# Kernel optimization log

Hardware: AMD Instinct MI355X
Metric: run time of the kernel (lower is better)

## Reference

```python
import jax, jax.numpy as jnp
import numpy as np

# module config (init_kwargs)
AH, AW = 14, 14            # aligned_height, aligned_width
SCALE = 0.25               # spatial_scale
RATIO = 2                  # sampling_ratio
SHIFT = 0.0                # spatial_shift (added in feature-map coords)
HALF_PART = 0              # 0 = full box
ROI_SCALE = 1.0            # box rescale about its center


def setup_inputs() -> dict:
    key = jax.random.key(0)
    kf, kb, kx, ky, kw, kh = jax.random.split(key, 6)
    B, C, H, W = 2, 256, 200, 272
    N = 256
    features = jax.random.normal(kf, (B, C, H, W), dtype=jnp.float32)
    img_h, img_w = H / SCALE, W / SCALE
    bidx = jax.random.randint(kb, (N,), 0, B).astype(jnp.float32)
    x1 = jax.random.uniform(kx, (N,)) * (img_w * 0.6)
    y1 = jax.random.uniform(ky, (N,)) * (img_h * 0.6)
    bw = 32.0 + jax.random.uniform(kw, (N,)) * (img_w * 0.35)
    bh = 32.0 + jax.random.uniform(kh, (N,)) * (img_h * 0.35)
    rois = jnp.stack([bidx, x1, y1, x1 + bw, y1 + bh], axis=1).astype(jnp.float32)
    return {"features": features, "rois": rois}


def _lin_idx(coord, size):
    # bilinear index/weight prep with RoIAlign boundary rules
    valid = (coord > -1.0) & (coord < float(size))
    c = jnp.clip(coord, 0.0, float(size - 1))
    lo = jnp.floor(c)
    hi = jnp.minimum(lo + 1.0, float(size - 1))
    frac = c - lo
    return lo.astype(jnp.int32), hi.astype(jnp.int32), frac, valid.astype(coord.dtype)


def _roi_mask_align(features, rois):
    B, C, H, W = features.shape
    N = rois.shape[0]
    PH, PW, r = AH + 1, AW + 1, RATIO
    b = rois[:, 0].astype(jnp.int32)
    # to feature-map coords, with roi_scale about the box center and spatial_shift
    x1, y1, x2, y2 = (rois[:, 1] * SCALE, rois[:, 2] * SCALE,
                      rois[:, 3] * SCALE, rois[:, 4] * SCALE)
    cx, cy = 0.5 * (x1 + x2), 0.5 * (y1 + y2)
    hw, hh = 0.5 * (x2 - x1) * ROI_SCALE, 0.5 * (y2 - y1) * ROI_SCALE
    x1, x2 = cx - hw + SHIFT, cx + hw + SHIFT
    y1, y2 = cy - hh + SHIFT, cy + hh + SHIFT
    roi_w = jnp.maximum(x2 - x1, 1.0)
    roi_h = jnp.maximum(y2 - y1, 1.0)
    bin_w = roi_w / PW
    bin_h = roi_h / PH
    # sample coords, separable: sx [N, PW*r], sy [N, PH*r]
    ix = jnp.arange(PW * r, dtype=jnp.float32)
    iy = jnp.arange(PH * r, dtype=jnp.float32)
    sx = x1[:, None] + (ix[None, :] + 0.5) * (bin_w[:, None] / r)
    sy = y1[:, None] + (iy[None, :] + 0.5) * (bin_h[:, None] / r)
    y_lo, y_hi, fy, vy = _lin_idx(sy, H)
    x_lo, x_hi, fx, vx = _lin_idx(sx, W)
    featsT = jnp.transpose(features, (0, 2, 3, 1))  # [B,H,W,C]
    bb = b[:, None, None]
    gather = lambda yi, xi: featsT[bb, yi[:, :, None], xi[:, None, :]]  # [N,Sy,Sx,C]
    wy0, wy1 = 1.0 - fy, fy
    wx0, wx1 = 1.0 - fx, fx
    val = (gather(y_lo, x_lo) * (wy0[:, :, None] * wx0[:, None, :])[..., None]
           + gather(y_lo, x_hi) * (wy0[:, :, None] * wx1[:, None, :])[..., None]
           + gather(y_hi, x_lo) * (wy1[:, :, None] * wx0[:, None, :])[..., None]
           + gather(y_hi, x_hi) * (wy1[:, :, None] * wx1[:, None, :])[..., None])
    val = val * (vy[:, :, None] * vx[:, None, :])[..., None]
    # average the r*r samples per bin -> [N, PH, PW, C]
    val = val.reshape(N, PH, r, PW, r, C).mean(axis=(2, 4))
    return jnp.transpose(val, (0, 3, 1, 2))  # [N, C, PH, PW]


def reference(features, rois):
    x = _roi_mask_align(features, rois)  # [N, C, AH+1, AW+1]
    # avg_pool2d(kernel=2, stride=1)
    out = 0.25 * (x[..., :-1, :-1] + x[..., 1:, :-1]
                  + x[..., :-1, 1:] + x[..., 1:, 1:])
    return out  # [N, C, AH, AW]
```

## Files before the change

### kernel.cpp

```cpp
#include <hip/hip_runtime.h>


#define AH_  14
#define AW_  14
#define C_   256
#define H_   200
#define W_   272
#define HW_  (H_ * W_)
#define CPB  4
#define WBUF 1424

#define GLOAD_LDS16(g, l)                                                     \
  __builtin_amdgcn_global_load_lds(                                           \
      (const __attribute__((address_space(1))) void*)(g),                     \
      (__attribute__((address_space(3))) void*)(l), 16, 0, 0)

__global__ __launch_bounds__(128)
void roi_mask_align_avg_kernel(const float* __restrict__ feat,
                               const float* __restrict__ rois,
                               float* __restrict__ out) {
    __shared__ float Ls[2][WBUF];

    const int p   = blockIdx.x;
    const int xcd = p & 7;
    const int q   = p >> 3;
    const int n   = q & 255;
    const int cgi = q >> 8;
    const int cg  = cgi * 8 + xcd;
    const int c0  = cg * CPB;

    const int tid  = threadIdx.x;
    const int wave = tid >> 6;
    const int lane = tid & 63;
    const int half = lane >> 5;
    const int ix   = lane & 31;

    float* __restrict__ LsW = Ls[wave];
    if (lane == 0) LsW[1024] = 0.0f;

    const float r0f = rois[n * 5 + 0];
    const float x1s = rois[n * 5 + 1] * 0.25f;
    const float y1s = rois[n * 5 + 2] * 0.25f;
    const float x2s = rois[n * 5 + 3] * 0.25f;
    const float y2s = rois[n * 5 + 4] * 0.25f;
    const int   b   = (int)r0f;

    const float cx = 0.5f * (x1s + x2s), cy = 0.5f * (y1s + y2s);
    const float hw = 0.5f * (x2s - x1s), hh = 0.5f * (y2s - y1s);
    const float x1 = cx - hw, x2 = cx + hw;
    const float y1 = cy - hh, y2 = cy + hh;
    const float roi_w = fmaxf(x2 - x1, 1.0f);
    const float roi_h = fmaxf(y2 - y1, 1.0f);
    const float sub_w = roi_w * (1.0f / 15.0f) * 0.5f;
    const float sub_h = roi_h * (1.0f / 15.0f) * 0.5f;

    const float sx  = x1 + ((float)ix + 0.5f) * sub_w;
    const bool  vx_ = (sx > -1.0f) && (sx < (float)W_) && (ix < 30);
    const float ccx = fminf(fmaxf(sx, 0.0f), (float)(W_ - 1));
    const float lox = floorf(ccx);
    const int   xl  = (int)lox;
    const int   xh  = min(xl + 1, W_ - 1);
    const float fx  = ccx - lox;
    const float vmx = vx_ ? 1.0f : 0.0f;
    const float wx0 = (1.0f - fx) * vmx;
    const float wx1 = fx * vmx;

    const int s0    = __builtin_amdgcn_readfirstlane(xl);
    const int s0c   = min(s0, W_ - 128);
    const int xh29  = __builtin_amdgcn_readlane(xh, 29);
    const int spanrel = xh29 - s0c;
    const bool ldact  = (ix * 4) <= spanrel;
    const int iA    = half * 128 + (xl - s0c);

    const float* __restrict__ bpA = feat + ((size_t)b * C_ + c0) * (size_t)HW_;
    const float* __restrict__ gA  = bpA + (size_t)half * HW_ + s0c + 4 * ix;
    const float* __restrict__ gB  = gA + 2 * HW_;

    const int  aw   = ix >> 1;
    const bool emit = ((lane & 1) == 0) && (aw < AW_);
    float* __restrict__ Ow = LsW + 1028;

    float alo0 = 0.f, alo1 = 0.f, ahi0 = 0.f, ahi1 = 0.f;
    float blo0 = 0.f, blo1 = 0.f, bhi0 = 0.f, bhi1 = 0.f;
    int   pyl = -100, pyh = -100;

    const int iy0 = wave * 14;
    float prevSA = 0.f, prevSB = 0.f;

    for (int kk = 0; kk < 8; ++kk) {
        float PA = 0.f, PB = 0.f;
        #pragma unroll
        for (int r = 0; r < 2; ++r) {
            const int iy = iy0 + 2 * kk + r;
            const float sy  = y1 + ((float)iy + 0.5f) * sub_h;
            const bool  vy_ = (sy > -1.0f) && (sy < (float)H_);
            const float ccy = fminf(fmaxf(sy, 0.0f), (float)(H_ - 1));
            const float loy = floorf(ccy);
            const float fy  = ccy - loy;
            const float vmy = vy_ ? 1.0f : 0.0f;
            const float wy0 = (1.0f - fy) * vmy;
            const float wy1 = fy * vmy;

            const int yl_s = __builtin_amdgcn_readfirstlane((int)loy);
            const int yh_s = min(yl_s + 1, H_ - 1);

            if (yl_s == pyl && yh_s == pyh) {
            } else if (yl_s == pyh) {
                alo0 = ahi0; alo1 = ahi1; blo0 = bhi0; blo1 = bhi1;
                const int ro = yh_s * W_;
                asm volatile("s_waitcnt lgkmcnt(0)" ::: "memory");
                if (ldact) {
                    GLOAD_LDS16(gA + ro, LsW + 512);
                    GLOAD_LDS16(gB + ro, LsW + 768);
                }
                asm volatile("s_waitcnt vmcnt(0)" ::: "memory");
                ahi0 = LsW[512 + iA]; ahi1 = LsW[512 + iA + 1];
                bhi0 = LsW[768 + iA]; bhi1 = LsW[768 + iA + 1];
            } else {
                const int rlo = yl_s * W_, rhi = yh_s * W_;
                asm volatile("s_waitcnt lgkmcnt(0)" ::: "memory");
                if (ldact) {
                    GLOAD_LDS16(gA + rlo, LsW + 0);
                    GLOAD_LDS16(gB + rlo, LsW + 256);
                    GLOAD_LDS16(gA + rhi, LsW + 512);
                    GLOAD_LDS16(gB + rhi, LsW + 768);
                }
                asm volatile("s_waitcnt vmcnt(0)" ::: "memory");
                alo0 = LsW[iA];       alo1 = LsW[iA + 1];
                blo0 = LsW[256 + iA]; blo1 = LsW[256 + iA + 1];
                ahi0 = LsW[512 + iA]; ahi1 = LsW[512 + iA + 1];
                bhi0 = LsW[768 + iA]; bhi1 = LsW[768 + iA + 1];
            }
            pyl = yl_s; pyh = yh_s;

            const float w00 = wy0 * wx0, w01 = wy0 * wx1;
            const float w10 = wy1 * wx0, w11 = wy1 * wx1;
            PA += alo0 * w00 + alo1 * w01 + ahi0 * w10 + ahi1 * w11;
            PB += blo0 * w00 + blo1 * w01 + bhi0 * w10 + bhi1 * w11;
        }
        const float tA = PA + __shfl_xor(PA, 1, 64);
        const float uA = tA + __shfl_down(tA, 2, 64);
        const float tB = PB + __shfl_xor(PB, 1, 64);
        const float uB = tB + __shfl_down(tB, 2, 64);
        if (kk > 0 && emit) {
            const int row = kk - 1;
            Ow[half * 98 + row * AW_ + aw]       = (prevSA + uA) * 0.0625f;
            Ow[(2 + half) * 98 + row * AW_ + aw] = (prevSB + uB) * 0.0625f;
        }
        prevSA = uA;
        prevSB = uB;
    }

    float* __restrict__ op = out + ((size_t)n * C_ + c0) * (AH_ * AW_);
    for (int o = lane; o < CPB * 7 * AW_; o += 64) {
        const int ch  = o / 98;
        const int rem = o - ch * 98;
        op[ch * (AH_ * AW_) + wave * 98 + rem] = Ow[o];
    }
}

extern "C" void kernel_launch(void* const* d_in, const int* in_sizes, int n_in,
                              void* d_out, int out_size, void* d_ws, size_t ws_size,
                              hipStream_t stream) {
    const float* feat = (const float*)d_in[0];
    const float* rois = (const float*)d_in[1];
    float* out = (float*)d_out;
    const int grid = 256 * (C_ / CPB);
    roi_mask_align_avg_kernel<<<grid, 128, 0, stream>>>(feat, rois, out);
}
```

Baseline: 233.5 us.

## Double-buffer row staging to overlap next-row global loads with current compute

Replaces the row-reuse branching loop with a fully unrolled 16-step loop. Each step prefetches the next sample row pair into an alternate LDS buffer using async global-to-LDS loads, then waits only on the older batch with vmcnt(4). Row reuse is dropped, so every sample row pair is reloaded, which adds memory traffic in exchange for hiding load latency. It also zero-fills a larger LDS region, shifts the second half-wave's load window left by 8 columns, and keeps the output rows in registers until the end.

```diff
diff --git a/kernel.cpp b/kernel.cpp
--- a/kernel.cpp
+++ b/kernel.cpp
@@ -8,7 +8,7 @@
 #define W_   272
 #define HW_  (H_ * W_)
 #define CPB  4
-#define WBUF 1424
+#define WBUF 2056
 
 #define GLOAD_LDS16(g, l)                                                     \
   __builtin_amdgcn_global_load_lds(                                           \
@@ -36,7 +36,12 @@
     const int ix   = lane & 31;
 
     float* __restrict__ LsW = Ls[wave];
-    if (lane == 0) LsW[1024] = 0.0f;
+    {
+        float4* L4 = (float4*)LsW;
+        for (int o = lane; o < WBUF / 4; o += 64)
+            L4[o] = make_float4(0.f, 0.f, 0.f, 0.f);
+    }
+    asm volatile("s_waitcnt lgkmcnt(0)" ::: "memory");
 
     const float r0f = rois[n * 5 + 0];
     const float x1s = rois[n * 5 + 1] * 0.25f;
@@ -66,96 +71,105 @@
     const float wx1 = fx * vmx;
 
     const int s0    = __builtin_amdgcn_readfirstlane(xl);
-    const int s0c   = min(s0, W_ - 128);
+    const int s0c0  = min(s0, W_ - 128);
+    const int s0c1  = max(min(s0 - 8, W_ - 128), 0);
+    const int s0ch  = half ? s0c1 : s0c0;
     const int xh29  = __builtin_amdgcn_readlane(xh, 29);
-    const int spanrel = xh29 - s0c;
-    const bool ldact  = (ix * 4) <= spanrel;
-    const int iA    = half * 128 + (xl - s0c);
+    const int spanh = xh29 - s0ch;
+    const bool ldact = (ix * 4) <= spanh;
+    const int iA    = half * 128 + (xl - s0ch);
 
     const float* __restrict__ bpA = feat + ((size_t)b * C_ + c0) * (size_t)HW_;
-    const float* __restrict__ gA  = bpA + (size_t)half * HW_ + s0c + 4 * ix;
-    const float* __restrict__ gB  = gA + 2 * HW_;
+    const float* __restrict__ gAl = bpA + (size_t)half * HW_ + s0ch + 4 * ix;
+    const float* __restrict__ gBl = gAl + 2 * HW_;
 
     const int  aw   = ix >> 1;
     const bool emit = ((lane & 1) == 0) && (aw < AW_);
-    float* __restrict__ Ow = LsW + 1028;
+    const int  iy0  = wave * 14;
 
-    float alo0 = 0.f, alo1 = 0.f, ahi0 = 0.f, ahi1 = 0.f;
-    float blo0 = 0.f, blo1 = 0.f, bhi0 = 0.f, bhi1 = 0.f;
-    int   pyl = -100, pyh = -100;
+    auto geom = [&](int iy, int& olo, int& ohi, float& wy0, float& wy1) {
+        const float sy  = y1 + ((float)iy + 0.5f) * sub_h;
+        const bool  vy_ = (sy > -1.0f) && (sy < (float)H_);
+        const float ccy = fminf(fmaxf(sy, 0.0f), (float)(H_ - 1));
+        const float loy = floorf(ccy);
+        const float fy  = ccy - loy;
+        const float vmy = vy_ ? 1.0f : 0.0f;
+        wy0 = (1.0f - fy) * vmy;
+        wy1 = fy * vmy;
+        const int yl_s = __builtin_amdgcn_readfirstlane((int)loy);
+        const int yh_s = min(yl_s + 1, H_ - 1);
+        olo = yl_s * W_;
+        ohi = yh_s * W_;
+    };
+    auto stage = [&](int bb, int olo, int ohi) {
+        float* d = LsW + bb * 1024;
+        if (ldact) {
+            GLOAD_LDS16(gAl + olo, d);
+            GLOAD_LDS16(gBl + olo, d + 256);
+            GLOAD_LDS16(gAl + ohi, d + 512);
+            GLOAD_LDS16(gBl + ohi, d + 768);
+        }
+    };
 
-    const int iy0 = wave * 14;
-    float prevSA = 0.f, prevSB = 0.f;
+    int   olo_c, ohi_c;  float wy0_c, wy1_c;
+    geom(iy0, olo_c, ohi_c, wy0_c, wy1_c);
+    stage(0, olo_c, ohi_c);
 
-    for (int kk = 0; kk < 8; ++kk) {
-        float PA = 0.f, PB = 0.f;
+    float outA[7], outB[7];
+    float prevSA = 0.f, prevSB = 0.f, PA = 0.f, PB = 0.f;
+
+    #pragma unroll
+    for (int i = 0; i < 16; ++i) {
+        int olo_n, ohi_n; float wy0_n, wy1_n;
+        geom(iy0 + i + 1, olo_n, ohi_n, wy0_n, wy1_n);
+
+        asm volatile("s_waitcnt lgkmcnt(0)" ::: "memory");
+
+        stage((i + 1) & 1, olo_n, ohi_n);
+
+        asm volatile("s_waitcnt vmcnt(4)" ::: "memory");
+
+        const float* d = LsW + (i & 1) * 1024;
+        const float alo0 = d[iA],       alo1 = d[iA + 1];
+        const float blo0 = d[256 + iA], blo1 = d[256 + iA + 1];
+        const float ahi0 = d[512 + iA], ahi1 = d[512 + iA + 1];
+        const float bhi0 = d[768 + iA], bhi1 = d[768 + iA + 1];
+
+        const float w00 = wy0_c * wx0, w01 = wy0_c * wx1;
+        const float w10 = wy1_c * wx0, w11 = wy1_c * wx1;
+        PA += alo0 * w00 + alo1 * w01 + ahi0 * w10 + ahi1 * w11;
+        PB += blo0 * w00 + blo1 * w01 + bhi0 * w10 + bhi1 * w11;
+
+        if (i & 1) {
+            const float tA = PA + __shfl_xor(PA, 1, 64);
+            const float uA = tA + __shfl_down(tA, 2, 64);
+            const float tB = PB + __shfl_xor(PB, 1, 64);
+            const float uB = tB + __shfl_down(tB, 2, 64);
+            const int kk = i >> 1;
+            if (kk > 0) {
+                outA[kk - 1] = (prevSA + uA) * 0.0625f;
+                outB[kk - 1] = (prevSB + uB) * 0.0625f;
+            }
+            prevSA = uA; prevSB = uB;
+            PA = 0.f; PB = 0.f;
+        }
+        olo_c = olo_n; ohi_c = ohi_n; wy0_c = wy0_n; wy1_c = wy1_n;
+    }
+
+    asm volatile("s_waitcnt vmcnt(0)" ::: "memory");
+    if (emit) {
         #pragma unroll
-        for (int r = 0; r < 2; ++r) {
-            const int iy = iy0 + 2 * kk + r;
-            const float sy  = y1 + ((float)iy + 0.5f) * sub_h;
-            const bool  vy_ = (sy > -1.0f) && (sy < (float)H_);
-            const float ccy = fminf(fmaxf(sy, 0.0f), (float)(H_ - 1));
-            const float loy = floorf(ccy);
-            const float fy  = ccy - loy;
-            const float vmy = vy_ ? 1.0f : 0.0f;
-            const float wy0 = (1.0f - fy) * vmy;
-            const float wy1 = fy * vmy;
-
-            const int yl_s = __builtin_amdgcn_readfirstlane((int)loy);
-            const int yh_s = min(yl_s + 1, H_ - 1);
-
-            if (yl_s == pyl && yh_s == pyh) {
-            } else if (yl_s == pyh) {
-                alo0 = ahi0; alo1 = ahi1; blo0 = bhi0; blo1 = bhi1;
-                const int ro = yh_s * W_;
-                asm volatile("s_waitcnt lgkmcnt(0)" ::: "memory");
-                if (ldact) {
-                    GLOAD_LDS16(gA + ro, LsW + 512);
-                    GLOAD_LDS16(gB + ro, LsW + 768);
-                }
-                asm volatile("s_waitcnt vmcnt(0)" ::: "memory");
-                ahi0 = LsW[512 + iA]; ahi1 = LsW[512 + iA + 1];
-                bhi0 = LsW[768 + iA]; bhi1 = LsW[768 + iA + 1];
-            } else {
-                const int rlo = yl_s * W_, rhi = yh_s * W_;
-                asm volatile("s_waitcnt lgkmcnt(0)" ::: "memory");
-                if (ldact) {
-                    GLOAD_LDS16(gA + rlo, LsW + 0);
-                    GLOAD_LDS16(gB + rlo, LsW + 256);
-                    GLOAD_LDS16(gA + rhi, LsW + 512);
-                    GLOAD_LDS16(gB + rhi, LsW + 768);
-                }
-                asm volatile("s_waitcnt vmcnt(0)" ::: "memory");
-                alo0 = LsW[iA];       alo1 = LsW[iA + 1];
-                blo0 = LsW[256 + iA]; blo1 = LsW[256 + iA + 1];
-                ahi0 = LsW[512 + iA]; ahi1 = LsW[512 + iA + 1];
-                bhi0 = LsW[768 + iA]; bhi1 = LsW[768 + iA + 1];
-            }
-            pyl = yl_s; pyh = yh_s;
-
-            const float w00 = wy0 * wx0, w01 = wy0 * wx1;
-            const float w10 = wy1 * wx0, w11 = wy1 * wx1;
-            PA += alo0 * w00 + alo1 * w01 + ahi0 * w10 + ahi1 * w11;
-            PB += blo0 * w00 + blo1 * w01 + bhi0 * w10 + bhi1 * w11;
+        for (int k = 0; k < 7; ++k) {
+            LsW[half * 98 + k * AW_ + aw]       = outA[k];
+            LsW[(2 + half) * 98 + k * AW_ + aw] = outB[k];
         }
-        const float tA = PA + __shfl_xor(PA, 1, 64);
-        const float uA = tA + __shfl_down(tA, 2, 64);
-        const float tB = PB + __shfl_xor(PB, 1, 64);
-        const float uB = tB + __shfl_down(tB, 2, 64);
-        if (kk > 0 && emit) {
-            const int row = kk - 1;
-            Ow[half * 98 + row * AW_ + aw]       = (prevSA + uA) * 0.0625f;
-            Ow[(2 + half) * 98 + row * AW_ + aw] = (prevSB + uB) * 0.0625f;
-        }
-        prevSA = uA;
-        prevSB = uB;
     }
 
     float* __restrict__ op = out + ((size_t)n * C_ + c0) * (AH_ * AW_);
     for (int o = lane; o < CPB * 7 * AW_; o += 64) {
         const int ch  = o / 98;
         const int rem = o - ch * 98;
-        op[ch * (AH_ * AW_) + wave * 98 + rem] = Ow[o];
+        op[ch * (AH_ * AW_) + wave * 98 + rem] = LsW[o];
     }
 }
 
```

Result: slower. 252.7 us (+8.2%).
